# Optimization experiments

Measured on AMD Instinct MI355X. Metric: run time of the kernel, lower is better.

## Reference

```python
import jax, jax.numpy as jnp
import numpy as np

B, CIN, COUT, H, W, K = 4, 128, 128, 128, 128, 3
KK = K * K


def setup_inputs() -> dict:
    key = jax.random.key(0)
    ks = jax.random.split(key, 6)
    return {
        "inp": jax.random.normal(ks[0], (B, CIN, H, W), jnp.float32),
        "feat": jax.random.normal(ks[1], (B, CIN, H, W), jnp.float32),
        # small offset-conv weights keep predicted offsets in a realistic few-pixel range
        "w_off": jax.random.normal(ks[2], (3 * KK, CIN, K, K), jnp.float32) * 0.01,
        "b_off": jnp.zeros((3 * KK,), jnp.float32),
        "w_dc": jax.random.normal(ks[3], (COUT, CIN, K, K), jnp.float32) * (1.0 / np.sqrt(CIN * KK)),
        "b_dc": jnp.zeros((COUT,), jnp.float32),
    }


def _conv3x3(x, w, b):
    # stride=1, padding=1, dilation=1, groups=1 (module defaults)
    y = jax.lax.conv_general_dilated(x, w, (1, 1), ((1, 1), (1, 1)),
                                     dimension_numbers=("NCHW", "OIHW", "NCHW"))
    return y + b[None, :, None, None]


def _modulated_deform_conv(x, offset, mask, w, b):
    # DCNv2: offset [B, 2*KK, H, W] interleaved (y, x) per kernel tap, mask [B, KK, H, W]
    b_, c, h, wd = x.shape
    ky = jnp.repeat(jnp.arange(K), K)  # kernel row index per tap, [KK]
    kx = jnp.tile(jnp.arange(K), K)    # kernel col index per tap, [KK]
    off = offset.reshape(b_, KK, 2, h, wd)
    # sampling positions: out_idx - pad + k*dilation + learned offset
    py = off[:, :, 0] + (jnp.arange(h)[None, None, :, None] + ky[None, :, None, None] - 1).astype(offset.dtype)
    px = off[:, :, 1] + (jnp.arange(wd)[None, None, None, :] + kx[None, :, None, None] - 1).astype(offset.dtype)
    y0 = jnp.floor(py)
    x0 = jnp.floor(px)
    ly = py - y0  # bilinear fractions (grad flows to offsets through these)
    lx = px - x0
    y0i = y0.astype(jnp.int32)
    x0i = x0.astype(jnp.int32)
    x_flat = x.reshape(b_, c, h * wd)

    def corner(yi, xi, wgt):
        valid = (yi >= 0) & (yi < h) & (xi >= 0) & (xi < wd)  # zero padding outside
        idx = jnp.clip(yi, 0, h - 1) * wd + jnp.clip(xi, 0, wd - 1)
        g = jnp.take_along_axis(x_flat, idx.reshape(b_, 1, -1), axis=2).reshape(b_, c, KK, h, wd)
        return g * (wgt * valid)[:, None]

    val = (corner(y0i,     x0i,     (1 - ly) * (1 - lx))
         + corner(y0i,     x0i + 1, (1 - ly) * lx)
         + corner(y0i + 1, x0i,     ly * (1 - lx))
         + corner(y0i + 1, x0i + 1, ly * lx))
    val = val * mask[:, None]  # modulation
    out = jnp.einsum("bckhw,ock->bohw", val, w.reshape(w.shape[0], c, KK))
    return out + b[None, :, None, None]


def reference(inp, feat, w_off, b_off, w_dc, b_dc):
    o = _conv3x3(feat, w_off, b_off)
    o1, o2, m = jnp.split(o, 3, axis=1)
    offset = jnp.concatenate([o1, o2], axis=1)
    mask = jax.nn.sigmoid(m)
    return _modulated_deform_conv(inp, offset, mask, w_dc, b_dc)
```

## Files before the change

### kernel.cpp

```cpp
#include <hip/hip_runtime.h>
#include <math.h>

#define B_    4
#define CIN_  128
#define COUT_ 128
#define H_    128
#define W_    128
#define HW_   (H_*W_)
#define KK_   9

typedef __attribute__((ext_vector_type(8))) short short8;
typedef __attribute__((ext_vector_type(4))) float f32x4;
typedef _Float16 h8 __attribute__((ext_vector_type(8)));
typedef float f2v __attribute__((ext_vector_type(2), aligned(4)));

static __device__ __forceinline__ unsigned short f2h(float f) {
    union { _Float16 h; unsigned short u; } v; v.h = (_Float16)f;
    return v.u;
}


__global__ __launch_bounds__(256) void prep_kernel(
    const float* __restrict__ inp, const float* __restrict__ feat,
    const float* __restrict__ w_dc, const float* __restrict__ w_off,
    unsigned short* __restrict__ inpT, unsigned short* __restrict__ featT,
    unsigned short* __restrict__ w_swz, unsigned short* __restrict__ woff_swz)
{
    const int bx = blockIdx.x;
    const int tid = threadIdx.x;
    __shared__ unsigned short s_T[128 * 142];

    if (bx < 1024) {
        const int bi = bx & 511;
        const int b = bi >> 7, y = bi & 127;
        const float* src = (bx < 512 ? inp : feat) + (size_t)b * CIN_ * HW_ + y * W_;
        unsigned short* dstb = (bx < 512 ? inpT : featT) + (size_t)bi * (W_ * CIN_);
        const int xs = (tid & 63) * 2;
        const int c0 = tid >> 6;
#pragma unroll 4
        for (int p = 0; p < 32; ++p) {
            int c = c0 + 4 * p;
            f2v d = *(const f2v*)(src + (size_t)c * HW_ + xs);
            s_T[xs * 142 + c]       = f2h(d.x);
            s_T[(xs + 1) * 142 + c] = f2h(d.y);
        }
        __syncthreads();
        const int cs = (tid & 15) * 8;
        const int x0 = tid >> 4;
#pragma unroll
        for (int p = 0; p < 8; ++p) {
            int x = x0 + 16 * p;
            unsigned r[4];
#pragma unroll
            for (int j = 0; j < 4; ++j) {
                unsigned lo = s_T[x * 142 + cs + 2 * j];
                unsigned hi = s_T[x * 142 + cs + 2 * j + 1];
                r[j] = lo | (hi << 16);
            }
            *(int4*)(dstb + (size_t)x * CIN_ + cs) = make_int4(r[0], r[1], r[2], r[3]);
        }
    } else if (bx < 1096) {
        int idx = (bx - 1024) * 256 + tid;
        int q   = idx >> 9;
        int rem = idx & 511;
        int ocb = rem >> 6;
        int l   = rem & 63;
        int cbq = q / 9;
        int k   = q - cbq * 9;
        int cb  = (cbq << 5) + ((l >> 4) << 3);
        int oc  = (ocb << 4) + (l & 15);
        unsigned r[4];
#pragma unroll
        for (int j = 0; j < 4; ++j) {
            float f0 = w_dc[((size_t)(oc * CIN_ + cb + 2 * j    )) * KK_ + k];
            float f1 = w_dc[((size_t)(oc * CIN_ + cb + 2 * j + 1)) * KK_ + k];
            r[j] = (unsigned)f2h(f0) | ((unsigned)f2h(f1) << 16);
        }
        *(int4*)&w_swz[(size_t)idx * 8] = make_int4(r[0], r[1], r[2], r[3]);
    } else {
        int idx = (bx - 1096) * 256 + tid;
        int q   = idx >> 7;
        int rem = idx & 127;
        int l   = rem & 63;
        int cbq = q / 9;
        int k   = q - cbq * 9;
        int cb  = (cbq << 5) + ((l >> 4) << 3);
        int oc  = ((rem >> 6) << 4) + (l & 15);
        unsigned r[4];
#pragma unroll
        for (int j = 0; j < 4; ++j) {
            float f0 = 0.f, f1 = 0.f;
            if (oc < 27) {
                f0 = w_off[((size_t)(oc * CIN_ + cb + 2 * j    )) * KK_ + k];
                f1 = w_off[((size_t)(oc * CIN_ + cb + 2 * j + 1)) * KK_ + k];
            }
            r[j] = (unsigned)f2h(f0) | ((unsigned)f2h(f1) << 16);
        }
        *(int4*)&woff_swz[(size_t)idx * 8] = make_int4(r[0], r[1], r[2], r[3]);
    }
}

__global__ __launch_bounds__(256, 4) void fused_kernel(
    const unsigned short* __restrict__ featT, const unsigned short* __restrict__ inpT,
    const unsigned short* __restrict__ woff_swz, const unsigned short* __restrict__ w_swz,
    const float* __restrict__ b_off, const float* __restrict__ b_dc,
    float* __restrict__ out)
{
    const int tid = threadIdx.x;
    const int bx = blockIdx.x;
    const int lidx = ((bx & 7) << 7) | (bx >> 3);
    const int b  = lidx >> 8;
    const int h  = (lidx & 255) >> 1;
    const int w0 = (lidx & 1) << 6;

    __shared__ __align__(16) unsigned short s_R0[7936];
    __shared__ float  offv[27][65];
    __shared__ int2   s_midx[576];
    __shared__ float4 s_mwgt[576];

    unsigned short (*s_F)[66][40] = (unsigned short (*)[66][40])s_R0;
    unsigned short (*s_V)[64][40] = (unsigned short (*)[64][40])s_R0;

    const int lane = tid & 63;
    const int wave = tid >> 6;
    const int kg = lane >> 4, pn = lane & 15;

    {
        const unsigned short* fT = featT;
        f32x4 acc[2];
        acc[0] = (f32x4){0.f, 0.f, 0.f, 0.f};
        acc[1] = (f32x4){0.f, 0.f, 0.f, 0.f};

        const int me = tid >> 2;
        const int mg = tid & 3;

        for (int cb = 0; cb < 4; ++cb) {
            if (cb) __syncthreads();

#pragma unroll
            for (int r = 0; r < 3; ++r) {
                int y = h + r - 1;
                h8 d{};
                if ((unsigned)y < (unsigned)H_)
                    d = *(const h8*)(fT + (((size_t)(b * H_ + y) * W_ + (w0 + me)) * CIN_
                                           + (cb << 5) + (mg << 3)));
                *(h8*)&s_F[r][me + 1][mg << 3] = d;
            }
            if (tid < 24) {
                int r = tid >> 3, side = (tid >> 2) & 1, g = tid & 3;
                int x = side ? (w0 + 64) : (w0 - 1);
                int t = side ? 65 : 0;
                int y = h + r - 1;
                h8 d{};
                if (((unsigned)y < (unsigned)H_) & ((unsigned)x < (unsigned)W_))
                    d = *(const h8*)(fT + (((size_t)(b * H_ + y) * W_ + x) * CIN_
                                           + (cb << 5) + (g << 3)));
                *(h8*)&s_F[r][t][g << 3] = d;
            }
            __syncthreads();

            const int qb2 = cb * 18;
            const h8* wb = (const h8*)woff_swz;
            h8 a0 = wb[(size_t)(qb2    ) * 64 + lane];
            h8 a1 = wb[(size_t)(qb2 + 1) * 64 + lane];
#pragma unroll
            for (int k = 0; k < 9; ++k) {
                const int ky = k / 3, kx = k - 3 * ky;
                h8 bfr = *(const h8*)&s_F[ky][wave * 16 + pn + kx][kg * 8];
                h8 na0, na1;
                if (k < 8) {
                    na0 = wb[(size_t)(qb2 + 2 * k + 2) * 64 + lane];
                    na1 = wb[(size_t)(qb2 + 2 * k + 3) * 64 + lane];
                }
                acc[0] = __builtin_amdgcn_mfma_f32_16x16x32_f16(a0, bfr, acc[0], 0, 0, 0);
                acc[1] = __builtin_amdgcn_mfma_f32_16x16x32_f16(a1, bfr, acc[1], 0, 0, 0);
                if (k < 8) { a0 = na0; a1 = na1; }
            }
        }

        const int row0 = (lane >> 4) << 2;
        const int col  = lane & 15;
        const int pwl  = wave * 16 + col;
#pragma unroll
        for (int mt = 0; mt < 2; ++mt) {
#pragma unroll
            for (int i = 0; i < 4; ++i) {
                int oc = mt * 16 + row0 + i;
                if (oc < 27) {
                    float v = acc[mt][i] + b_off[oc];
                    if (oc >= 18) v = 1.f / (1.f + __expf(-v));
                    offv[oc][pwl] = v;
                }
            }
        }
    }
    __syncthreads();

    for (int i = tid; i < 576; i += 256) {
        int k = i >> 6, p = i & 63;
        int ky = k / 3, kx = k - ky * 3;
        int pw = w0 + p;
        float offy = offv[2 * k    ][p];
        float offx = offv[2 * k + 1][p];
        float mask = offv[18 + k   ][p];
        float py  = offy + (float)(h  + ky - 1);
        float px_ = offx + (float)(pw + kx - 1);
        float y0f = floorf(py), x0f = floorf(px_);
        float ly = py - y0f, lx = px_ - x0f;
        int y0 = (int)y0f, x0 = (int)x0f;
        int y1 = y0 + 1;
        int hx = min(max(x0, 0), W_ - 2);
        float wlo = 0.f, whi = 0.f;
        if (x0 == hx)          { wlo = 1.f - lx; whi = lx; }
        else if (x0 == hx - 1) { wlo = lx; }
        else if (x0 == hx + 1) { whi = 1.f - lx; }
        float wt_top = ((unsigned)y0 < (unsigned)H_) ? (1.f - ly) * mask : 0.f;
        float wt_bot = ((unsigned)y1 < (unsigned)H_) ? ly * mask : 0.f;
        int cy0 = min(max(y0, 0), H_ - 1), cy1 = min(max(y1, 0), H_ - 1);
        s_midx[i] = make_int2(cy0 * W_ + hx, cy1 * W_ + hx);
        s_mwgt[i] = make_float4(wt_top * wlo, wt_top * whi,
                                wt_bot * wlo, wt_bot * whi);
    }
    __syncthreads();

    const int px = tid >> 2;
    const int cs = tid & 3;
    const char* inpTb = (const char*)(inpT + (size_t)b * CIN_ * HW_);

    f32x4 acc2[2][4];
#pragma unroll
    for (int mt = 0; mt < 2; ++mt)
#pragma unroll
        for (int nt = 0; nt < 4; ++nt) acc2[mt][nt] = (f32x4){0.f, 0.f, 0.f, 0.f};

    h8 pf0, pf1, pf2, pf3;

    auto issue = [&](int qq) {
        int cbq = qq / 9;
        int k   = qq - cbq * 9;
        int2 id = s_midx[(k << 6) + px];
        int coff = (cbq << 6) + (cs << 4);
        const char* g0 = inpTb + ((size_t)(unsigned)id.x << 8) + coff;
        const char* g1 = inpTb + ((size_t)(unsigned)id.y << 8) + coff;
        pf0 = *(const h8*)(g0);
        pf1 = *(const h8*)(g0 + 256);
        pf2 = *(const h8*)(g1);
        pf3 = *(const h8*)(g1 + 256);
    };

    issue(0);
    const h8* wp0 = (const h8*)w_swz + (size_t)(wave * 2) * 64 + lane;
    h8 af0 = wp0[0];
    h8 af1 = wp0[64];

    for (int q = 0; q < 36; ++q) {
        int k = q - (q / 9) * 9;

        float4 wt = s_mwgt[(k << 6) + px];
        h8 v = pf0 * (_Float16)wt.x;
        v += pf1 * (_Float16)wt.y;
        v += pf2 * (_Float16)wt.z;
        v += pf3 * (_Float16)wt.w;

        *(h8*)&s_V[q & 1][px][cs << 3] = v;

        int qn = (q + 1 < 36) ? q + 1 : 35;
        issue(qn);
        const h8* wpn = (const h8*)w_swz + (size_t)(qn * 8 + wave * 2) * 64 + lane;
        h8 na0 = wpn[0];
        h8 na1 = wpn[64];

        asm volatile("s_waitcnt lgkmcnt(0)" ::: "memory");
        __builtin_amdgcn_s_barrier();
        __builtin_amdgcn_sched_barrier(0);

#pragma unroll
        for (int nt = 0; nt < 4; ++nt) {
            h8 bfr = *(const h8*)&s_V[q & 1][nt * 16 + pn][kg * 8];
            acc2[0][nt] = __builtin_amdgcn_mfma_f32_16x16x32_f16(af0, bfr, acc2[0][nt], 0, 0, 0);
            acc2[1][nt] = __builtin_amdgcn_mfma_f32_16x16x32_f16(af1, bfr, acc2[1][nt], 0, 0, 0);
        }
        af0 = na0; af1 = na1;
    }

    const int row0 = (lane >> 4) << 2;
    const int col  = lane & 15;
#pragma unroll
    for (int mt = 0; mt < 2; ++mt) {
#pragma unroll
        for (int nt = 0; nt < 4; ++nt) {
            int pw = w0 + nt * 16 + col;
#pragma unroll
            for (int i = 0; i < 4; ++i) {
                int oc = wave * 32 + mt * 16 + row0 + i;
                out[((size_t)(b * COUT_ + oc)) * HW_ + h * W_ + pw] =
                    acc2[mt][nt][i] + b_dc[oc];
            }
        }
    }
}

extern "C" void kernel_launch(void* const* d_in, const int* in_sizes, int n_in,
                              void* d_out, int out_size, void* d_ws, size_t ws_size,
                              hipStream_t stream)
{
    const float* inp   = (const float*)d_in[0];
    const float* feat  = (const float*)d_in[1];
    const float* w_off = (const float*)d_in[2];
    const float* b_off = (const float*)d_in[3];
    const float* w_dc  = (const float*)d_in[4];
    const float* b_dc  = (const float*)d_in[5];
    float* out  = (float*)d_out;
    unsigned short* w_swz    = (unsigned short*)d_ws;
    unsigned short* woff_swz = (unsigned short*)((char*)d_ws + 294912);
    unsigned short* inpT     = (unsigned short*)((char*)d_ws + 368640);
    unsigned short* featT    = (unsigned short*)((char*)d_ws + 368640 + 16777216);

    prep_kernel<<<dim3(1114), dim3(256), 0, stream>>>(inp, feat, w_dc, w_off,
                                                      inpT, featT, w_swz, woff_swz);
    fused_kernel<<<dim3(1024), dim3(256), 0, stream>>>(featT, inpT, woff_swz, w_swz,
                                                       b_off, b_dc, out);
}
```

Before: 163.8 us.

## Feed sampled values directly as MFMA B-operand, dropping LDS staging and barriers

The deformable-conv main loop now lays threads out so that each wave builds the bilinear-sampled column fragment in registers in exactly the MFMA B-operand layout (16 pixels x 32 channels per wave). Each wave then multiplies it against all 8 output-channel tiles. This removes the LDS write/read of the sampled tile and the per-iteration block barrier. In exchange each wave must load all 8 weight A-fragments per step from global/L2 instead of 2, with no prefetch, so weight traffic per wave rises fourfold and load latency may be exposed.

```diff
diff --git a/kernel.cpp b/kernel.cpp
--- a/kernel.cpp
+++ b/kernel.cpp
@@ -9,7 +9,6 @@
 #define HW_   (H_*W_)
 #define KK_   9
 
-typedef __attribute__((ext_vector_type(8))) short short8;
 typedef __attribute__((ext_vector_type(4))) float f32x4;
 typedef _Float16 h8 __attribute__((ext_vector_type(8)));
 typedef float f2v __attribute__((ext_vector_type(2), aligned(4)));
@@ -119,7 +118,6 @@
     __shared__ float4 s_mwgt[576];
 
     unsigned short (*s_F)[66][40] = (unsigned short (*)[66][40])s_R0;
-    unsigned short (*s_V)[64][40] = (unsigned short (*)[64][40])s_R0;
 
     const int lane = tid & 63;
     const int wave = tid >> 6;
@@ -178,9 +176,8 @@
             }
         }
 
-        const int row0 = (lane >> 4) << 2;
-        const int col  = lane & 15;
-        const int pwl  = wave * 16 + col;
+        const int row0 = kg << 2;
+        const int pwl  = wave * 16 + pn;
 #pragma unroll
         for (int mt = 0; mt < 2; ++mt) {
 #pragma unroll
@@ -223,23 +220,20 @@
     }
     __syncthreads();
 
-    const int px = tid >> 2;
-    const int cs = tid & 3;
+    const int p = wave * 16 + pn;
     const char* inpTb = (const char*)(inpT + (size_t)b * CIN_ * HW_);
 
-    f32x4 acc2[2][4];
-#pragma unroll
-    for (int mt = 0; mt < 2; ++mt)
-#pragma unroll
-        for (int nt = 0; nt < 4; ++nt) acc2[mt][nt] = (f32x4){0.f, 0.f, 0.f, 0.f};
+    f32x4 acc2[8];
+#pragma unroll
+    for (int m = 0; m < 8; ++m) acc2[m] = (f32x4){0.f, 0.f, 0.f, 0.f};
 
     h8 pf0, pf1, pf2, pf3;
 
     auto issue = [&](int qq) {
         int cbq = qq / 9;
         int k   = qq - cbq * 9;
-        int2 id = s_midx[(k << 6) + px];
-        int coff = (cbq << 6) + (cs << 4);
+        int2 id = s_midx[(k << 6) + p];
+        int coff = (cbq << 6) + (kg << 4);
         const char* g0 = inpTb + ((size_t)(unsigned)id.x << 8) + coff;
         const char* g1 = inpTb + ((size_t)(unsigned)id.y << 8) + coff;
         pf0 = *(const h8*)(g0);
@@ -249,53 +243,35 @@
     };
 
     issue(0);
-    const h8* wp0 = (const h8*)w_swz + (size_t)(wave * 2) * 64 + lane;
-    h8 af0 = wp0[0];
-    h8 af1 = wp0[64];
 
     for (int q = 0; q < 36; ++q) {
         int k = q - (q / 9) * 9;
 
-        float4 wt = s_mwgt[(k << 6) + px];
+        float4 wt = s_mwgt[(k << 6) + p];
         h8 v = pf0 * (_Float16)wt.x;
         v += pf1 * (_Float16)wt.y;
         v += pf2 * (_Float16)wt.z;
         v += pf3 * (_Float16)wt.w;
 
-        *(h8*)&s_V[q & 1][px][cs << 3] = v;
-
         int qn = (q + 1 < 36) ? q + 1 : 35;
         issue(qn);
-        const h8* wpn = (const h8*)w_swz + (size_t)(qn * 8 + wave * 2) * 64 + lane;
-        h8 na0 = wpn[0];
-        h8 na1 = wpn[64];
-
-        asm volatile("s_waitcnt lgkmcnt(0)" ::: "memory");
-        __builtin_amdgcn_s_barrier();
-        __builtin_amdgcn_sched_barrier(0);
-
-#pragma unroll
-        for (int nt = 0; nt < 4; ++nt) {
-            h8 bfr = *(const h8*)&s_V[q & 1][nt * 16 + pn][kg * 8];
-            acc2[0][nt] = __builtin_amdgcn_mfma_f32_16x16x32_f16(af0, bfr, acc2[0][nt], 0, 0, 0);
-            acc2[1][nt] = __builtin_amdgcn_mfma_f32_16x16x32_f16(af1, bfr, acc2[1][nt], 0, 0, 0);
-        }
-        af0 = na0; af1 = na1;
-    }
-
-    const int row0 = (lane >> 4) << 2;
-    const int col  = lane & 15;
-#pragma unroll
-    for (int mt = 0; mt < 2; ++mt) {
-#pragma unroll
-        for (int nt = 0; nt < 4; ++nt) {
-            int pw = w0 + nt * 16 + col;
-#pragma unroll
-            for (int i = 0; i < 4; ++i) {
-                int oc = wave * 32 + mt * 16 + row0 + i;
-                out[((size_t)(b * COUT_ + oc)) * HW_ + h * W_ + pw] =
-                    acc2[mt][nt][i] + b_dc[oc];
-            }
+
+        const h8* wp = (const h8*)w_swz + (size_t)(q * 8) * 64 + lane;
+#pragma unroll
+        for (int m = 0; m < 8; ++m) {
+            h8 af = wp[(size_t)m * 64];
+            acc2[m] = __builtin_amdgcn_mfma_f32_16x16x32_f16(af, v, acc2[m], 0, 0, 0);
+        }
+    }
+
+    const int pw = w0 + wave * 16 + pn;
+#pragma unroll
+    for (int m = 0; m < 8; ++m) {
+#pragma unroll
+        for (int i = 0; i < 4; ++i) {
+            int oc = m * 16 + (kg << 2) + i;
+            out[((size_t)(b * COUT_ + oc)) * HW_ + h * W_ + pw] =
+                acc2[m][i] + b_dc[oc];
         }
     }
 }
```

Result: slower. 217.9 us (+33.0%).

## Reorder deform gather loop tap-outer, channel-block-inner and pad s_V rows

Applied to the files above, without the earlier changes.

The main loop now iterates taps outermost and the four channel blocks innermost, so each tap's sampling index and bilinear weights are read from LDS once and the gather addresses are reused with small channel offsets. This trims per-step LDS index loads and address arithmetic. Weight-fragment indexing is adjusted to match the new order. The s_V row stride is padded from 40 to 44 halfs to cut LDS bank conflicts on the B-fragment reads, at the cost of a slightly larger shared footprint inside the existing aliased buffer.

```diff
diff --git a/kernel.cpp b/kernel.cpp
--- a/kernel.cpp
+++ b/kernel.cpp
@@ -9,7 +9,6 @@
 #define HW_   (H_*W_)
 #define KK_   9
 
-typedef __attribute__((ext_vector_type(8))) short short8;
 typedef __attribute__((ext_vector_type(4))) float f32x4;
 typedef _Float16 h8 __attribute__((ext_vector_type(8)));
 typedef float f2v __attribute__((ext_vector_type(2), aligned(4)));
@@ -119,7 +118,7 @@
     __shared__ float4 s_mwgt[576];
 
     unsigned short (*s_F)[66][40] = (unsigned short (*)[66][40])s_R0;
-    unsigned short (*s_V)[64][40] = (unsigned short (*)[64][40])s_R0;
+    unsigned short (*s_V)[64][44] = (unsigned short (*)[64][44])s_R0;
 
     const int lane = tid & 63;
     const int wave = tid >> 6;
@@ -178,9 +177,8 @@
             }
         }
 
-        const int row0 = (lane >> 4) << 2;
-        const int col  = lane & 15;
-        const int pwl  = wave * 16 + col;
+        const int row0 = kg << 2;
+        const int pwl  = wave * 16 + pn;
 #pragma unroll
         for (int mt = 0; mt < 2; ++mt) {
 #pragma unroll
@@ -235,52 +233,70 @@
 
     h8 pf0, pf1, pf2, pf3;
 
-    auto issue = [&](int qq) {
-        int cbq = qq / 9;
-        int k   = qq - cbq * 9;
-        int2 id = s_midx[(k << 6) + px];
-        int coff = (cbq << 6) + (cs << 4);
-        const char* g0 = inpTb + ((size_t)(unsigned)id.x << 8) + coff;
-        const char* g1 = inpTb + ((size_t)(unsigned)id.y << 8) + coff;
-        pf0 = *(const h8*)(g0);
-        pf1 = *(const h8*)(g0 + 256);
-        pf2 = *(const h8*)(g1);
-        pf3 = *(const h8*)(g1 + 256);
-    };
-
-    issue(0);
-    const h8* wp0 = (const h8*)w_swz + (size_t)(wave * 2) * 64 + lane;
-    h8 af0 = wp0[0];
-    h8 af1 = wp0[64];
-
-    for (int q = 0; q < 36; ++q) {
-        int k = q - (q / 9) * 9;
-
-        float4 wt = s_mwgt[(k << 6) + px];
-        h8 v = pf0 * (_Float16)wt.x;
-        v += pf1 * (_Float16)wt.y;
-        v += pf2 * (_Float16)wt.z;
-        v += pf3 * (_Float16)wt.w;
-
-        *(h8*)&s_V[q & 1][px][cs << 3] = v;
-
-        int qn = (q + 1 < 36) ? q + 1 : 35;
-        issue(qn);
-        const h8* wpn = (const h8*)w_swz + (size_t)(qn * 8 + wave * 2) * 64 + lane;
-        h8 na0 = wpn[0];
-        h8 na1 = wpn[64];
-
-        asm volatile("s_waitcnt lgkmcnt(0)" ::: "memory");
-        __builtin_amdgcn_s_barrier();
-        __builtin_amdgcn_sched_barrier(0);
-
-#pragma unroll
-        for (int nt = 0; nt < 4; ++nt) {
-            h8 bfr = *(const h8*)&s_V[q & 1][nt * 16 + pn][kg * 8];
-            acc2[0][nt] = __builtin_amdgcn_mfma_f32_16x16x32_f16(af0, bfr, acc2[0][nt], 0, 0, 0);
-            acc2[1][nt] = __builtin_amdgcn_mfma_f32_16x16x32_f16(af1, bfr, acc2[1][nt], 0, 0, 0);
-        }
-        af0 = na0; af1 = na1;
+    int2 id0 = s_midx[px];
+    float4 wt = s_mwgt[px];
+    const char* g0 = inpTb + ((size_t)(unsigned)id0.x << 8) + (cs << 4);
+    const char* g1 = inpTb + ((size_t)(unsigned)id0.y << 8) + (cs << 4);
+    pf0 = *(const h8*)(g0);
+    pf1 = *(const h8*)(g0 + 256);
+    pf2 = *(const h8*)(g1);
+    pf3 = *(const h8*)(g1 + 256);
+
+    h8 af0, af1;
+    {
+        const h8* wp = (const h8*)w_swz + (size_t)(wave * 2) * 64 + lane;
+        af0 = wp[0];
+        af1 = wp[64];
+    }
+
+    for (int k = 0; k < 9; ++k) {
+        const int kn = (k + 1 < 9) ? k + 1 : 8;
+        int2 idn = s_midx[(kn << 6) + px];
+        float4 wtn = s_mwgt[(kn << 6) + px];
+        const char* g0n = inpTb + ((size_t)(unsigned)idn.x << 8) + (cs << 4);
+        const char* g1n = inpTb + ((size_t)(unsigned)idn.y << 8) + (cs << 4);
+
+#pragma unroll
+        for (int cbq = 0; cbq < 4; ++cbq) {
+            h8 v = pf0 * (_Float16)wt.x;
+            v += pf1 * (_Float16)wt.y;
+            v += pf2 * (_Float16)wt.z;
+            v += pf3 * (_Float16)wt.w;
+
+            const int par = cbq & 1;
+            *(h8*)&s_V[par][px][cs << 3] = v;
+
+            if (cbq < 3) {
+                const int off = (cbq + 1) << 6;
+                pf0 = *(const h8*)(g0 + off);
+                pf1 = *(const h8*)(g0 + 256 + off);
+                pf2 = *(const h8*)(g1 + off);
+                pf3 = *(const h8*)(g1 + 256 + off);
+            } else {
+                pf0 = *(const h8*)(g0n);
+                pf1 = *(const h8*)(g0n + 256);
+                pf2 = *(const h8*)(g1n);
+                pf3 = *(const h8*)(g1n + 256);
+            }
+
+            const int qn = (cbq < 3) ? (cbq + 1) * 9 + k : kn;
+            const h8* wpn = (const h8*)w_swz + (size_t)(qn * 8 + wave * 2) * 64 + lane;
+            h8 na0 = wpn[0];
+            h8 na1 = wpn[64];
+
+            asm volatile("s_waitcnt lgkmcnt(0)" ::: "memory");
+            __builtin_amdgcn_s_barrier();
+            __builtin_amdgcn_sched_barrier(0);
+
+#pragma unroll
+            for (int nt = 0; nt < 4; ++nt) {
+                h8 bfr = *(const h8*)&s_V[par][nt * 16 + pn][kg * 8];
+                acc2[0][nt] = __builtin_amdgcn_mfma_f32_16x16x32_f16(af0, bfr, acc2[0][nt], 0, 0, 0);
+                acc2[1][nt] = __builtin_amdgcn_mfma_f32_16x16x32_f16(af1, bfr, acc2[1][nt], 0, 0, 0);
+            }
+            af0 = na0; af1 = na1;
+        }
+        g0 = g0n; g1 = g1n; wt = wtn;
     }
 
     const int row0 = (lane >> 4) << 2;
```

Result: slower. 211.2 us (+28.9%).
